# Kernel optimization log

Hardware: AMD Instinct MI355X
Metric: run time of the kernel (lower is better)

Reference implementation:

```python
import jax, jax.numpy as jnp
import numpy as np

BITS = 4
GROUP_SIZE = 128
IN_FEATURES = 4096
OUT_FEATURES = 11008
BATCH = 128


def setup_inputs() -> dict:
    key = jax.random.key(0)
    k1, k2, k3, k4 = jax.random.split(key, 4)
    x = jax.random.normal(k1, (BATCH, IN_FEATURES), dtype=jnp.float32)
    # packed 4-bit weights: each int32 holds 8 nibbles along the in-feature dim
    qweight = jax.random.randint(k2, (IN_FEATURES // 32 * BITS, OUT_FEATURES), 0, 2147483647, dtype=jnp.int32)
    n_groups = IN_FEATURES // GROUP_SIZE
    scales = jax.random.uniform(k3, (n_groups, OUT_FEATURES), dtype=jnp.float32) * 0.01 + 1e-3
    # note: in GPTQLinear_woo, `zeros` buffer already stores scale*zero_point
    zeros = jax.random.normal(k4, (n_groups, OUT_FEATURES), dtype=jnp.float32) * 0.01
    return {"x": x, "qweight": qweight, "scales": scales, "zeros": zeros}


def _dequant(qweight, scales, zeros):
    out_f = qweight.shape[1]
    shifts = jnp.arange(0, 32, BITS, dtype=jnp.int32)  # [8]
    # [in/8, 8, out] -> unpack nibbles (mask kills arithmetic-shift sign bits)
    w = (qweight[:, None, :] >> shifts[None, :, None]) & (2 ** BITS - 1)
    w = w.reshape(-1, GROUP_SIZE, out_f).astype(scales.dtype)  # [n_groups, gs, out]
    w = scales[:, None, :] * w - zeros[:, None, :]
    return w.reshape(-1, out_f)  # [in, out]


def reference(x, qweight, scales, zeros):
    w = _dequant(qweight, scales, zeros)
    return jnp.matmul(x, w)  # [batch, out]
```

## Files before the change

kernel.cpp:

```cpp
#include <hip/hip_runtime.h>
#include <hip/hip_bf16.h>
#include <stdint.h>


#define IN_F   4096
#define OUT_F  11008
#define BATCH  128
#define BK     64
#define BN     64
#define NCHUNK (IN_F / BK)
#define SPLIT  8
#define KSC    (NCHUNK / SPLIT)
#define NBLK   (OUT_F / BN)
#define MN     (BATCH * OUT_F)

typedef __attribute__((ext_vector_type(8))) short short8;
typedef __attribute__((ext_vector_type(4))) float f32x4;

static __device__ __forceinline__ unsigned int f2bf_pack(float lo, float hi) {
  unsigned int a = __float_as_uint(lo);
  unsigned int b = __float_as_uint(hi);
  a += 0x7FFFu + ((a >> 16) & 1u);
  b += 0x7FFFu + ((b >> 16) & 1u);
  return (a >> 16) | (b & 0xFFFF0000u);
}

__global__ __launch_bounds__(256) void cvt_kernel(const float* __restrict__ x,
                                                  unsigned int* __restrict__ xb) {
  int i = blockIdx.x * 256 + threadIdx.x;
  float4 v0 = *(const float4*)(x + (size_t)i * 8);
  float4 v1 = *(const float4*)(x + (size_t)i * 8 + 4);
  uint4 o;
  o.x = f2bf_pack(v0.x, v0.y);
  o.y = f2bf_pack(v0.z, v0.w);
  o.z = f2bf_pack(v1.x, v1.y);
  o.w = f2bf_pack(v1.z, v1.w);
  *(uint4*)(xb + (size_t)i * 4) = o;
}

__global__ __launch_bounds__(256) void zero_out(float* __restrict__ out) {
  int base = (blockIdx.x * 256 + threadIdx.x) * 16;
  float4 z = {0.f, 0.f, 0.f, 0.f};
#pragma unroll
  for (int j = 0; j < 4; ++j) *(float4*)(out + base + j * 4) = z;
}

__global__ __launch_bounds__(256) void reduce_kernel(const float* __restrict__ part,
                                                     float* __restrict__ out) {
  int base = (blockIdx.x * 256 + threadIdx.x) * 8;
  float4 s0 = {0.f, 0.f, 0.f, 0.f}, s1 = s0;
#pragma unroll
  for (int s = 0; s < SPLIT; ++s) {
    const float* p = part + (size_t)s * MN + base;
    float4 a = *(const float4*)(p);
    float4 b = *(const float4*)(p + 4);
    s0.x += a.x; s0.y += a.y; s0.z += a.z; s0.w += a.w;
    s1.x += b.x; s1.y += b.y; s1.z += b.z; s1.w += b.w;
  }
  *(float4*)(out + base)     = s0;
  *(float4*)(out + base + 4) = s1;
}

#define LOAD_CHUNK(AP, QP, CH) do {                                            \
    const int k0_ = (CH) * BK;                                                 \
    _Pragma("unroll")                                                          \
    for (int i_ = 0; i_ < 4; ++i_) {                                           \
      int seg_ = tid + 256 * i_, row_ = seg_ >> 3, sc_ = seg_ & 7;             \
      if (use_xb) {                                                            \
        AP[i_] = *(const uint4*)(xb + (size_t)row_ * IN_F + k0_ + sc_ * 8);    \
      } else {                                                                 \
        const float* p_ = x + (size_t)row_ * IN_F + k0_ + sc_ * 8;             \
        float4 u0_ = *(const float4*)(p_);                                     \
        float4 u1_ = *(const float4*)(p_ + 4);                                 \
        AP[i_].x = f2bf_pack(u0_.x, u0_.y);                                    \
        AP[i_].y = f2bf_pack(u0_.z, u0_.w);                                    \
        AP[i_].z = f2bf_pack(u1_.x, u1_.y);                                    \
        AP[i_].w = f2bf_pack(u1_.z, u1_.w);                                    \
      }                                                                        \
    }                                                                          \
    _Pragma("unroll")                                                          \
    for (int i_ = 0; i_ < 2; ++i_) {                                           \
      QP[i_] = (unsigned int)qweight[(size_t)(k0_ / 8 + wid + 4 * i_) * OUT_F  \
                                     + n0 + col];                              \
    }                                                                          \
  } while (0)

#define STORE_CHUNK(AP, QP, CC) do {                                           \
    _Pragma("unroll")                                                          \
    for (int i_ = 0; i_ < 4; ++i_) {                                           \
      int seg_ = tid + 256 * i_, row_ = seg_ >> 3, sc_ = seg_ & 7;             \
      *(uint4*)(aLds + row_ * 128 + ((sc_ * 16) ^ ((row_ & 7) << 4))) = AP[i_];\
    }                                                                          \
    {                                                                          \
      float s_ = sreg[(CC) >> 1], z_ = zreg[(CC) >> 1];                        \
      _Pragma("unroll")                                                        \
      for (int i_ = 0; i_ < 2; ++i_) {                                         \
        unsigned int q_ = QP[i_];                                              \
        int qr_ = wid + 4 * i_;                                                \
        float f0_ = s_ * (float)((q_ >> 0)  & 0xFu) - z_;                      \
        float f1_ = s_ * (float)((q_ >> 4)  & 0xFu) - z_;                      \
        float f2_ = s_ * (float)((q_ >> 8)  & 0xFu) - z_;                      \
        float f3_ = s_ * (float)((q_ >> 12) & 0xFu) - z_;                      \
        float f4_ = s_ * (float)((q_ >> 16) & 0xFu) - z_;                      \
        float f5_ = s_ * (float)((q_ >> 20) & 0xFu) - z_;                      \
        float f6_ = s_ * (float)((q_ >> 24) & 0xFu) - z_;                      \
        float f7_ = s_ * (float)((q_ >> 28) & 0xFu) - z_;                      \
        uint4 v_;                                                              \
        v_.x = f2bf_pack(f0_, f1_);                                            \
        v_.y = f2bf_pack(f2_, f3_);                                            \
        v_.z = f2bf_pack(f4_, f5_);                                            \
        v_.w = f2bf_pack(f6_, f7_);                                            \
        *(uint4*)(bLds + col * 128 + ((qr_ * 16) ^ ((col & 7) << 4))) = v_;    \
      }                                                                        \
    }                                                                          \
  } while (0)

__global__ __launch_bounds__(256) void gptq_gemm(
    const unsigned short* __restrict__ xb,
    const float* __restrict__ x,
    const int* __restrict__ qweight,
    const float* __restrict__ scales,
    const float* __restrict__ zeros,
    float* __restrict__ outp,
    int use_xb, int atomic_mode) {
  __shared__ char aLds[BATCH * 128];
  __shared__ char bLds[BN * 128];

  const int tid  = threadIdx.x;
  const int lane = tid & 63;
  const int wid  = tid >> 6;
  const int wr   = wid >> 1;
  const int wc   = wid & 1;
  const int nb   = blockIdx.x % NBLK;
  const int sl   = blockIdx.x / NBLK;
  const int n0   = nb * BN;
  const int c0   = sl * KSC;

  float* dst = atomic_mode ? outp : outp + (size_t)sl * MN;

  const int col = tid & 63;
  const int g0  = c0 >> 1;
  float sreg[KSC / 2], zreg[KSC / 2];
#pragma unroll
  for (int g = 0; g < KSC / 2; ++g) {
    sreg[g] = scales[(size_t)(g0 + g) * OUT_F + n0 + col];
    zreg[g] = zeros [(size_t)(g0 + g) * OUT_F + n0 + col];
  }

  uint4 aP0[4], aP1[4];
  unsigned int qP0[2], qP1[2];
  LOAD_CHUNK(aP0, qP0, c0);
  LOAD_CHUNK(aP1, qP1, c0 + 1);

  f32x4 acc[4][2] = {};

#pragma unroll
  for (int cc = 0; cc < KSC; ++cc) {
    __syncthreads();

    if ((cc & 1) == 0) {
      STORE_CHUNK(aP0, qP0, cc);
      if (cc + 2 < KSC) LOAD_CHUNK(aP0, qP0, c0 + cc + 2);
    } else {
      STORE_CHUNK(aP1, qP1, cc);
      if (cc + 2 < KSC) LOAD_CHUNK(aP1, qP1, c0 + cc + 2);
    }
    __syncthreads();

#pragma unroll
    for (int ks = 0; ks < 2; ++ks) {
      int kbyte = ks * 64 + ((lane >> 4) << 4);
      short8 bfrag[2];
#pragma unroll
      for (int ct = 0; ct < 2; ++ct) {
        int c = wc * 32 + ct * 16 + (lane & 15);
        bfrag[ct] = *(const short8*)(bLds + c * 128 + (kbyte ^ ((c & 7) << 4)));
      }
#pragma unroll
      for (int rt = 0; rt < 4; ++rt) {
        int row = wr * 64 + rt * 16 + (lane & 15);
        short8 afrag = *(const short8*)(aLds + row * 128 + (kbyte ^ ((row & 7) << 4)));
#pragma unroll
        for (int ct = 0; ct < 2; ++ct) {
          acc[rt][ct] = __builtin_amdgcn_mfma_f32_16x16x32_bf16(afrag, bfrag[ct], acc[rt][ct], 0, 0, 0);
        }
      }
    }
  }

#pragma unroll
  for (int rt = 0; rt < 4; ++rt) {
#pragma unroll
    for (int ct = 0; ct < 2; ++ct) {
      int c = n0 + wc * 32 + ct * 16 + (lane & 15);
#pragma unroll
      for (int r = 0; r < 4; ++r) {
        int row = wr * 64 + rt * 16 + ((lane >> 4) << 2) + r;
        if (atomic_mode) {
          atomicAdd(dst + (size_t)row * OUT_F + c, acc[rt][ct][r]);
        } else {
          dst[(size_t)row * OUT_F + c] = acc[rt][ct][r];
        }
      }
    }
  }
}

extern "C" void kernel_launch(void* const* d_in, const int* in_sizes, int n_in,
                              void* d_out, int out_size, void* d_ws, size_t ws_size,
                              hipStream_t stream) {
  const float* x       = (const float*)d_in[0];
  const int*   qweight = (const int*)d_in[1];
  const float* scales  = (const float*)d_in[2];
  const float* zeros   = (const float*)d_in[3];
  float*       outp    = (float*)d_out;

  const size_t xb_bytes   = (size_t)BATCH * IN_F * sizeof(unsigned short);
  const size_t part_bytes = (size_t)SPLIT * MN * sizeof(float);
  int use_xb   = (ws_size >= xb_bytes) ? 1 : 0;
  int partials = (ws_size >= xb_bytes + part_bytes) ? 1 : 0;

  unsigned short* xb   = (unsigned short*)d_ws;
  float*          part = (float*)((char*)d_ws + xb_bytes);

  if (use_xb) {
    cvt_kernel<<<256, 256, 0, stream>>>(x, (unsigned int*)d_ws);
  }

  if (partials) {
    gptq_gemm<<<NBLK * SPLIT, 256, 0, stream>>>(xb, x, qweight, scales, zeros,
                                                part, use_xb, 0);
    reduce_kernel<<<688, 256, 0, stream>>>(part, outp);
  } else {
    zero_out<<<344, 256, 0, stream>>>(outp);
    gptq_gemm<<<NBLK * SPLIT, 256, 0, stream>>>(xb, x, qweight, scales, zeros,
                                                outp, use_xb, 1);
  }
}
```

Before: 44.43 us.

## Double-buffer LDS tiles with one barrier per step and halve K-split

Shared memory for the A and B tiles is doubled so the next chunk is dequantized and stored into one buffer while MFMAs read the other. This cuts the two barriers per K-step down to one. Quantized-weight loads are now prefetched three chunks ahead through a rotating register set. The K-split factor drops from 8 to 4, which halves the partial-sum traffic and the reduce work. The cost is fewer blocks in flight, longer per-block loops, and more LDS and registers per block, which may lower occupancy.

```diff
diff --git a/kernel.cpp b/kernel.cpp
--- a/kernel.cpp
+++ b/kernel.cpp
@@ -9,7 +9,7 @@
 #define BK     64
 #define BN     64
 #define NCHUNK (IN_F / BK)
-#define SPLIT  8
+#define SPLIT  4
 #define KSC    (NCHUNK / SPLIT)
 #define NBLK   (OUT_F / BN)
 #define MN     (BATCH * OUT_F)
@@ -61,41 +61,47 @@
   *(float4*)(out + base + 4) = s1;
 }
 
-#define LOAD_CHUNK(AP, QP, CH) do {                                            \
+#define LOAD_A(SET, CH) do {                                                   \
     const int k0_ = (CH) * BK;                                                 \
     _Pragma("unroll")                                                          \
     for (int i_ = 0; i_ < 4; ++i_) {                                           \
       int seg_ = tid + 256 * i_, row_ = seg_ >> 3, sc_ = seg_ & 7;             \
       if (use_xb) {                                                            \
-        AP[i_] = *(const uint4*)(xb + (size_t)row_ * IN_F + k0_ + sc_ * 8);    \
+        aP[SET][i_] = *(const uint4*)(xb + (size_t)row_ * IN_F + k0_ + sc_ * 8);\
       } else {                                                                 \
         const float* p_ = x + (size_t)row_ * IN_F + k0_ + sc_ * 8;             \
         float4 u0_ = *(const float4*)(p_);                                     \
         float4 u1_ = *(const float4*)(p_ + 4);                                 \
-        AP[i_].x = f2bf_pack(u0_.x, u0_.y);                                    \
-        AP[i_].y = f2bf_pack(u0_.z, u0_.w);                                    \
-        AP[i_].z = f2bf_pack(u1_.x, u1_.y);                                    \
-        AP[i_].w = f2bf_pack(u1_.z, u1_.w);                                    \
-      }                                                                        \
-    }                                                                          \
+        aP[SET][i_].x = f2bf_pack(u0_.x, u0_.y);                               \
+        aP[SET][i_].y = f2bf_pack(u0_.z, u0_.w);                               \
+        aP[SET][i_].z = f2bf_pack(u1_.x, u1_.y);                               \
+        aP[SET][i_].w = f2bf_pack(u1_.z, u1_.w);                               \
+      }                                                                        \
+    }                                                                          \
+  } while (0)
+
+#define LOAD_Q(SET, CH) do {                                                   \
+    const int k0_ = (CH) * BK;                                                 \
     _Pragma("unroll")                                                          \
     for (int i_ = 0; i_ < 2; ++i_) {                                           \
-      QP[i_] = (unsigned int)qweight[(size_t)(k0_ / 8 + wid + 4 * i_) * OUT_F  \
-                                     + n0 + col];                              \
-    }                                                                          \
-  } while (0)
-
-#define STORE_CHUNK(AP, QP, CC) do {                                           \
+      qP[SET][i_] = (unsigned int)qweight[(size_t)(k0_ / 8 + wid + 4 * i_) * OUT_F \
+                                          + n0 + col];                         \
+    }                                                                          \
+  } while (0)
+
+#define STORE_CHUNK(PB, AS, QS, GI) do {                                       \
+    char* aB_ = aLds + (PB) * (BATCH * 128);                                   \
+    char* bB_ = bLds + (PB) * (BN * 128);                                      \
     _Pragma("unroll")                                                          \
     for (int i_ = 0; i_ < 4; ++i_) {                                           \
       int seg_ = tid + 256 * i_, row_ = seg_ >> 3, sc_ = seg_ & 7;             \
-      *(uint4*)(aLds + row_ * 128 + ((sc_ * 16) ^ ((row_ & 7) << 4))) = AP[i_];\
+      *(uint4*)(aB_ + row_ * 128 + ((sc_ * 16) ^ ((row_ & 7) << 4))) = aP[AS][i_];\
     }                                                                          \
     {                                                                          \
-      float s_ = sreg[(CC) >> 1], z_ = zreg[(CC) >> 1];                        \
+      float s_ = sreg[GI], z_ = zreg[GI];                                      \
       _Pragma("unroll")                                                        \
       for (int i_ = 0; i_ < 2; ++i_) {                                         \
-        unsigned int q_ = QP[i_];                                              \
+        unsigned int q_ = qP[QS][i_];                                          \
         int qr_ = wid + 4 * i_;                                                \
         float f0_ = s_ * (float)((q_ >> 0)  & 0xFu) - z_;                      \
         float f1_ = s_ * (float)((q_ >> 4)  & 0xFu) - z_;                      \
@@ -110,7 +116,32 @@
         v_.y = f2bf_pack(f2_, f3_);                                            \
         v_.z = f2bf_pack(f4_, f5_);                                            \
         v_.w = f2bf_pack(f6_, f7_);                                            \
-        *(uint4*)(bLds + col * 128 + ((qr_ * 16) ^ ((col & 7) << 4))) = v_;    \
+        *(uint4*)(bB_ + col * 128 + ((qr_ * 16) ^ ((col & 7) << 4))) = v_;     \
+      }                                                                        \
+    }                                                                          \
+  } while (0)
+
+#define COMPUTE(PB) do {                                                       \
+    const char* aB_ = aLds + (PB) * (BATCH * 128);                             \
+    const char* bB_ = bLds + (PB) * (BN * 128);                                \
+    _Pragma("unroll")                                                          \
+    for (int ks_ = 0; ks_ < 2; ++ks_) {                                        \
+      int kb_ = ks_ * 64 + ((lane >> 4) << 4);                                 \
+      short8 bf_[2];                                                           \
+      _Pragma("unroll")                                                        \
+      for (int ct_ = 0; ct_ < 2; ++ct_) {                                      \
+        int c_ = wc * 32 + ct_ * 16 + (lane & 15);                             \
+        bf_[ct_] = *(const short8*)(bB_ + c_ * 128 + (kb_ ^ ((c_ & 7) << 4))); \
+      }                                                                        \
+      _Pragma("unroll")                                                        \
+      for (int rt_ = 0; rt_ < 4; ++rt_) {                                      \
+        int r_ = wr * 64 + rt_ * 16 + (lane & 15);                             \
+        short8 af_ = *(const short8*)(aB_ + r_ * 128 + (kb_ ^ ((r_ & 7) << 4)));\
+        _Pragma("unroll")                                                      \
+        for (int ct_ = 0; ct_ < 2; ++ct_) {                                    \
+          acc[rt_][ct_] = __builtin_amdgcn_mfma_f32_16x16x32_bf16(             \
+              af_, bf_[ct_], acc[rt_][ct_], 0, 0, 0);                          \
+        }                                                                      \
       }                                                                        \
     }                                                                          \
   } while (0)
@@ -123,8 +154,8 @@
     const float* __restrict__ zeros,
     float* __restrict__ outp,
     int use_xb, int atomic_mode) {
-  __shared__ char aLds[BATCH * 128];
-  __shared__ char bLds[BN * 128];
+  __shared__ char aLds[2 * BATCH * 128];
+  __shared__ char bLds[2 * BN * 128];
 
   const int tid  = threadIdx.x;
   const int lane = tid & 63;
@@ -147,45 +178,27 @@
     zreg[g] = zeros [(size_t)(g0 + g) * OUT_F + n0 + col];
   }
 
-  uint4 aP0[4], aP1[4];
-  unsigned int qP0[2], qP1[2];
-  LOAD_CHUNK(aP0, qP0, c0);
-  LOAD_CHUNK(aP1, qP1, c0 + 1);
+  uint4 aP[2][4];
+  unsigned int qP[3][2];
+
+  LOAD_A(0, c0);
+  LOAD_A(1, c0 + 1);
+  LOAD_Q(0, c0);
+  LOAD_Q(1, c0 + 1);
+  LOAD_Q(2, c0 + 2);
+  STORE_CHUNK(0, 0, 0, 0);
+  __syncthreads();
 
   f32x4 acc[4][2] = {};
 
 #pragma unroll
   for (int cc = 0; cc < KSC; ++cc) {
-    __syncthreads();
-
-    if ((cc & 1) == 0) {
-      STORE_CHUNK(aP0, qP0, cc);
-      if (cc + 2 < KSC) LOAD_CHUNK(aP0, qP0, c0 + cc + 2);
-    } else {
-      STORE_CHUNK(aP1, qP1, cc);
-      if (cc + 2 < KSC) LOAD_CHUNK(aP1, qP1, c0 + cc + 2);
-    }
-    __syncthreads();
-
-#pragma unroll
-    for (int ks = 0; ks < 2; ++ks) {
-      int kbyte = ks * 64 + ((lane >> 4) << 4);
-      short8 bfrag[2];
-#pragma unroll
-      for (int ct = 0; ct < 2; ++ct) {
-        int c = wc * 32 + ct * 16 + (lane & 15);
-        bfrag[ct] = *(const short8*)(bLds + c * 128 + (kbyte ^ ((c & 7) << 4)));
-      }
-#pragma unroll
-      for (int rt = 0; rt < 4; ++rt) {
-        int row = wr * 64 + rt * 16 + (lane & 15);
-        short8 afrag = *(const short8*)(aLds + row * 128 + (kbyte ^ ((row & 7) << 4)));
-#pragma unroll
-        for (int ct = 0; ct < 2; ++ct) {
-          acc[rt][ct] = __builtin_amdgcn_mfma_f32_16x16x32_bf16(afrag, bfrag[ct], acc[rt][ct], 0, 0, 0);
-        }
-      }
-    }
+    const int p = cc & 1;
+    if (cc + 2 < KSC) LOAD_A(p, c0 + cc + 2);
+    if (cc + 3 < KSC) LOAD_Q((cc) % 3, c0 + cc + 3);
+    if (cc + 1 < KSC) STORE_CHUNK(p ^ 1, p ^ 1, (cc + 1) % 3, (cc + 1) >> 1);
+    COMPUTE(p);
+    if (cc + 1 < KSC) __syncthreads();
   }
 
 #pragma unroll
```

New measurement: 40.78 us. 8.2% less time.
